# Performance work log

Measured on AMD Instinct MI355X. Metric: run time of the kernel, lower is better.

The kernel has to match this reference:

```python
import jax, jax.numpy as jnp
import numpy as np

N_NODES = 10000
N_EDGES = 640000
D_IN = 128
D_INTER = 128


def gcn_conv(x, edge_index, edge_weight, W, b):
    # PyG GCNConv: out = D^{-1/2} (A + I) D^{-1/2} (X W) + b
    n = x.shape[0]
    h = x @ W  # [N, D_out]
    row, col = edge_index[0], edge_index[1]  # source, target
    loop = jnp.arange(n, dtype=row.dtype)
    row = jnp.concatenate([row, loop])
    col = jnp.concatenate([col, loop])
    ew = jnp.concatenate([edge_weight, jnp.ones((n,), edge_weight.dtype)])
    deg = jax.ops.segment_sum(ew, col, num_segments=n)  # in-degree incl. self loops
    dinv = jnp.where(deg > 0, jax.lax.rsqrt(deg), jnp.zeros_like(deg))
    norm = dinv[row] * ew * dinv[col]  # [E+N]
    msgs = norm[:, None] * h[row]  # gather + scale
    out = jax.ops.segment_sum(msgs, col, num_segments=n)  # scatter-add aggregate
    return out + b


def setup_inputs() -> dict:
    key = jax.random.key(0)
    ks = jax.random.split(key, 8)
    x = jax.random.normal(ks[0], (N_NODES, D_IN), dtype=jnp.float32)
    edge_index = jax.random.randint(ks[1], (2, N_EDGES), 0, N_NODES, dtype=jnp.int64)
    edge_weight = jax.random.uniform(ks[2], (N_EDGES,), dtype=jnp.float32)
    # Glorot-ish init for linear weights, zeros for bias (PyG default)
    s1 = 1.0 / np.sqrt(D_IN)
    s2 = 1.0 / np.sqrt(D_INTER)
    W1 = jax.random.uniform(ks[3], (D_IN, D_INTER), jnp.float32, -s1, s1)
    b1 = jnp.zeros((D_INTER,), jnp.float32)
    W2 = jax.random.uniform(ks[4], (D_INTER, D_IN), jnp.float32, -s2, s2)
    b2 = jnp.zeros((D_IN,), jnp.float32)
    return {"x": x, "edge_index": edge_index, "edge_weight": edge_weight,
            "W1": W1, "b1": b1, "W2": W2, "b2": b2}


def reference(x, edge_index, edge_weight, W1, b1, W2, b2):
    # GCN.forward in eval mode: dropout is identity
    h = jax.nn.relu(gcn_conv(x, edge_index, edge_weight, W1, b1))
    out = jax.nn.relu(gcn_conv(h, edge_index, edge_weight, W2, b2))
    return out
```

## Files before the change

### kernel.cpp

```cpp
#include <hip/hip_runtime.h>

#define NN 10000
#define NE 640000
#define D  128
#define PAD_SHIFT 7
#define GEMM_BLOCKS ((NN + 31) / 32)
#define COUNT_BLOCKS (NE / 1024)


__global__ __launch_bounds__(256) void zero_kernel(int* __restrict__ p, int n) {
    int i = blockIdx.x * 256 + threadIdx.x;
    if (i < n) p[i] = 0;
}


__global__ __launch_bounds__(256) void fused_gemm_cs_kernel(const float* __restrict__ X,
                                                            const float* __restrict__ W,
                                                            float* __restrict__ H,
                                                            const int* __restrict__ ei,
                                                            const float* __restrict__ ew,
                                                            int* __restrict__ cnt,
                                                            int2* __restrict__ epack) {
    int bid = blockIdx.x;
    if (bid < GEMM_BLOCKS) {
        __shared__ float xs[32][D];
        int t  = threadIdx.x;
        int d  = t & 127;
        int rh = t >> 7;
        int r0 = bid * 32;
#pragma unroll
        for (int r = 0; r < 16; ++r) {
            int rr = r0 + rh * 16 + r;
            xs[rh * 16 + r][d] = (rr < NN) ? X[(size_t)rr * D + d] : 0.0f;
        }
        __syncthreads();
        float acc[16];
#pragma unroll
        for (int r = 0; r < 16; ++r) acc[r] = 0.0f;
        for (int k = 0; k < D; k += 4) {
            float w0 = W[(k + 0) * D + d];
            float w1 = W[(k + 1) * D + d];
            float w2 = W[(k + 2) * D + d];
            float w3 = W[(k + 3) * D + d];
#pragma unroll
            for (int r = 0; r < 16; ++r) {
                float4 xv = *reinterpret_cast<const float4*>(&xs[rh * 16 + r][k]);
                acc[r] = fmaf(xv.x, w0, acc[r]);
                acc[r] = fmaf(xv.y, w1, acc[r]);
                acc[r] = fmaf(xv.z, w2, acc[r]);
                acc[r] = fmaf(xv.w, w3, acc[r]);
            }
        }
#pragma unroll
        for (int r = 0; r < 16; ++r) {
            int rr = r0 + rh * 16 + r;
            if (rr < NN) H[(size_t)rr * D + d] = acc[r];
        }
    } else {
        int e0 = (bid - GEMM_BLOCKS) * 1024 + threadIdx.x;
        int   c[4], s[4];
        float w[4];
#pragma unroll
        for (int k = 0; k < 4; ++k) {
            int e = e0 + k * 256;
            c[k] = ei[NE + e];
            s[k] = ei[e];
            w[k] = ew[e];
        }
        int lr[4];
#pragma unroll
        for (int k = 0; k < 4; ++k) lr[k] = atomicAdd(&cnt[c[k]], 1);
#pragma unroll
        for (int k = 0; k < 4; ++k) {
            if (lr[k] < (1 << PAD_SHIFT)) {
                int2 v;
                v.x = s[k];
                v.y = __float_as_int(w[k]);
                epack[((size_t)c[k] << PAD_SHIFT) + lr[k]] = v;
            }
        }
    }
}


__global__ __launch_bounds__(256) void degdinv_kernel(const int* __restrict__ cnt,
                                                      const int2* __restrict__ epack,
                                                      float* __restrict__ dinv) {
    int node = blockIdx.x * 4 + (threadIdx.x >> 6);
    if (node >= NN) return;
    int lane = threadIdx.x & 63;
    int m = min(cnt[node], 1 << PAD_SHIFT);
    const int2* eb = epack + ((size_t)node << PAD_SHIFT);
    float s = 0.0f;
    for (int j = lane; j < m; j += 64) s += __int_as_float(eb[j].y);
#pragma unroll
    for (int off = 32; off; off >>= 1) s += __shfl_down(s, off);
    if (lane == 0) dinv[node] = rsqrtf(s + 1.0f);
}


__global__ __launch_bounds__(256) void gemm_kernel(const float* __restrict__ X,
                                                   const float* __restrict__ W,
                                                   float* __restrict__ H) {
    __shared__ float xs[32][D];
    int t  = threadIdx.x;
    int d  = t & 127;
    int rh = t >> 7;
    int r0 = blockIdx.x * 32;
#pragma unroll
    for (int r = 0; r < 16; ++r) {
        int rr = r0 + rh * 16 + r;
        xs[rh * 16 + r][d] = (rr < NN) ? X[(size_t)rr * D + d] : 0.0f;
    }
    __syncthreads();
    float acc[16];
#pragma unroll
    for (int r = 0; r < 16; ++r) acc[r] = 0.0f;
    for (int k = 0; k < D; k += 4) {
        float w0 = W[(k + 0) * D + d];
        float w1 = W[(k + 1) * D + d];
        float w2 = W[(k + 2) * D + d];
        float w3 = W[(k + 3) * D + d];
#pragma unroll
        for (int r = 0; r < 16; ++r) {
            float4 xv = *reinterpret_cast<const float4*>(&xs[rh * 16 + r][k]);
            acc[r] = fmaf(xv.x, w0, acc[r]);
            acc[r] = fmaf(xv.y, w1, acc[r]);
            acc[r] = fmaf(xv.z, w2, acc[r]);
            acc[r] = fmaf(xv.w, w3, acc[r]);
        }
    }
#pragma unroll
    for (int r = 0; r < 16; ++r) {
        int rr = r0 + rh * 16 + r;
        if (rr < NN) H[(size_t)rr * D + d] = acc[r];
    }
}


__global__ __launch_bounds__(64) void agg_half_kernel(const float* __restrict__ H,
                                                      const int* __restrict__ cnt,
                                                      const int2* __restrict__ epack,
                                                      const float* __restrict__ dinv,
                                                      const float* __restrict__ bias,
                                                      float* __restrict__ out) {
    __shared__ int   s_src[128];
    __shared__ float s_n[128];
    int i    = blockIdx.x;
    int slot = i & 7;
    int hh   = slot & 1;
    int c    = (i >> 3) * 4 + (slot >> 1);
    int t    = threadIdx.x;
    int d    = (hh << 6) | t;
    int m    = min(cnt[c], 1 << PAD_SHIFT);
    const int2* eb = epack + ((size_t)c << PAD_SHIFT);
    float di = dinv[c];
    for (int j = t; j < m; j += 64) {
        int2 v = eb[j];
        s_src[j] = v.x;
        s_n[j]   = dinv[v.x] * __int_as_float(v.y);
    }
    __syncthreads();
    float acc = di * H[(size_t)c * D + d];
    int jj = 0;
    for (; jj + 8 <= m; jj += 8) {
#pragma unroll
        for (int k = 0; k < 8; ++k)
            acc = fmaf(s_n[jj + k], H[(size_t)s_src[jj + k] * D + d], acc);
    }
    for (; jj < m; ++jj)
        acc = fmaf(s_n[jj], H[(size_t)s_src[jj] * D + d], acc);
    out[(size_t)c * D + d] = fmaxf(fmaf(di, acc, bias[d]), 0.0f);
}


extern "C" void kernel_launch(void* const* d_in, const int* in_sizes, int n_in,
                              void* d_out, int out_size, void* d_ws, size_t ws_size,
                              hipStream_t stream) {
    const float* x  = (const float*)d_in[0];
    const int*   ei = (const int*)  d_in[1];
    const float* ew = (const float*)d_in[2];
    const float* W1 = (const float*)d_in[3];
    const float* b1 = (const float*)d_in[4];
    const float* W2 = (const float*)d_in[5];
    const float* b2 = (const float*)d_in[6];
    float* out = (float*)d_out;

    char* ws = (char*)d_ws;
    size_t off = 0;
    auto alloc = [&](size_t bytes) {
        void* p = ws + off;
        off = (off + bytes + 255) & ~(size_t)255;
        return p;
    };
    int*   cnt   = (int*)  alloc(NN * 4);
    float* dinv  = (float*)alloc(NN * 4);
    int2*  epack = (int2*) alloc(((size_t)NN << PAD_SHIFT) * 8);
    float* h     = (float*)alloc((size_t)NN * D * 4);
    float* g     = (float*)alloc((size_t)NN * D * 4);

    zero_kernel<<<(NN + 255) / 256, 256, 0, stream>>>(cnt, NN);
    fused_gemm_cs_kernel<<<GEMM_BLOCKS + COUNT_BLOCKS, 256, 0, stream>>>(
        x, W1, h, ei, ew, cnt, epack);
    degdinv_kernel<<<(NN + 3) / 4, 256, 0, stream>>>(cnt, epack, dinv);

    agg_half_kernel<<<NN * 2, 64, 0, stream>>>(h, cnt, epack, dinv, b1, g);
    gemm_kernel    <<<(NN + 31) / 32, 256, 0, stream>>>(g, W2, h);
    agg_half_kernel<<<NN * 2, 64, 0, stream>>>(h, cnt, epack, dinv, b2, out);
}
```

Before: 137.6 us.

## Build edge buckets via per-block shared-memory histograms with batched global atomics

Replaces the per-edge global atomicAdd on the destination counters with a two-pass scheme. Each of 32 large blocks first histograms its edge slice in LDS, then reserves slot ranges with one global atomic per node, then scatters the edges into the padded buckets. The GEMM half of the fused kernel moves to 1024-thread blocks with fewer rows per thread so both roles can share one LDS union. This cuts global atomic contention, but the edge-building work now runs on only 32 blocks and reads the edge list twice. Local ranks are packed into 8 bits, which assumes no node receives more than 255 edges within one block's slice.

Measured after the change: 516.5 us. 275% more time.

```diff
diff --git a/kernel.cpp b/kernel.cpp
--- a/kernel.cpp
+++ b/kernel.cpp
@@ -4,8 +4,10 @@
 #define NE 640000
 #define D  128
 #define PAD_SHIFT 7
-#define GEMM_BLOCKS ((NN + 31) / 32)
-#define COUNT_BLOCKS (NE / 1024)
+#define GEMM_BLOCKS 313
+#define HIST_BLOCKS 32
+#define EPB (NE / HIST_BLOCKS)
+#define HSIZE 10240
 
 
 __global__ __launch_bounds__(256) void zero_kernel(int* __restrict__ p, int n) {
@@ -14,37 +16,39 @@
 }
 
 
-__global__ __launch_bounds__(256) void fused_gemm_cs_kernel(const float* __restrict__ X,
-                                                            const float* __restrict__ W,
-                                                            float* __restrict__ H,
-                                                            const int* __restrict__ ei,
-                                                            const float* __restrict__ ew,
-                                                            int* __restrict__ cnt,
-                                                            int2* __restrict__ epack) {
+union UShared {
+    float xs[32][D];
+    int   lh[HSIZE];
+};
+
+__global__ __launch_bounds__(1024) void fused_build_kernel(const float* __restrict__ X,
+                                                           const float* __restrict__ W,
+                                                           float* __restrict__ H,
+                                                           const int* __restrict__ ei,
+                                                           const float* __restrict__ ew,
+                                                           int* __restrict__ cnt,
+                                                           int2* __restrict__ epack) {
+    __shared__ UShared u;
     int bid = blockIdx.x;
+    int t   = threadIdx.x;
     if (bid < GEMM_BLOCKS) {
-        __shared__ float xs[32][D];
-        int t  = threadIdx.x;
         int d  = t & 127;
-        int rh = t >> 7;
+        int rg = t >> 7;
         int r0 = bid * 32;
-#pragma unroll
-        for (int r = 0; r < 16; ++r) {
-            int rr = r0 + rh * 16 + r;
-            xs[rh * 16 + r][d] = (rr < NN) ? X[(size_t)rr * D + d] : 0.0f;
-        }
-        __syncthreads();
-        float acc[16];
-#pragma unroll
-        for (int r = 0; r < 16; ++r) acc[r] = 0.0f;
+        for (int r = rg; r < 32; r += 8) {
+            int rr = r0 + r;
+            u.xs[r][d] = (rr < NN) ? X[(size_t)rr * D + d] : 0.0f;
+        }
+        __syncthreads();
+        float acc[4] = {0.f, 0.f, 0.f, 0.f};
         for (int k = 0; k < D; k += 4) {
             float w0 = W[(k + 0) * D + d];
             float w1 = W[(k + 1) * D + d];
             float w2 = W[(k + 2) * D + d];
             float w3 = W[(k + 3) * D + d];
 #pragma unroll
-            for (int r = 0; r < 16; ++r) {
-                float4 xv = *reinterpret_cast<const float4*>(&xs[rh * 16 + r][k]);
+            for (int r = 0; r < 4; ++r) {
+                float4 xv = *reinterpret_cast<const float4*>(&u.xs[rg * 4 + r][k]);
                 acc[r] = fmaf(xv.x, w0, acc[r]);
                 acc[r] = fmaf(xv.y, w1, acc[r]);
                 acc[r] = fmaf(xv.z, w2, acc[r]);
@@ -52,31 +56,37 @@
             }
         }
 #pragma unroll
-        for (int r = 0; r < 16; ++r) {
-            int rr = r0 + rh * 16 + r;
+        for (int r = 0; r < 4; ++r) {
+            int rr = r0 + rg * 4 + r;
             if (rr < NN) H[(size_t)rr * D + d] = acc[r];
         }
     } else {
-        int e0 = (bid - GEMM_BLOCKS) * 1024 + threadIdx.x;
-        int   c[4], s[4];
-        float w[4];
-#pragma unroll
-        for (int k = 0; k < 4; ++k) {
-            int e = e0 + k * 256;
-            c[k] = ei[NE + e];
-            s[k] = ei[e];
-            w[k] = ew[e];
-        }
-        int lr[4];
-#pragma unroll
-        for (int k = 0; k < 4; ++k) lr[k] = atomicAdd(&cnt[c[k]], 1);
-#pragma unroll
-        for (int k = 0; k < 4; ++k) {
-            if (lr[k] < (1 << PAD_SHIFT)) {
+        int bh = bid - GEMM_BLOCKS;
+        int e0 = bh * EPB;
+        for (int i = t; i < HSIZE; i += 1024) u.lh[i] = 0;
+        __syncthreads();
+        unsigned lrp[5] = {0u, 0u, 0u, 0u, 0u};
+        for (int j = t, k = 0; j < EPB; j += 1024, ++k) {
+            int c  = ei[NE + e0 + j];
+            int lr = atomicAdd(&u.lh[c], 1);
+            lrp[k >> 2] |= (unsigned)(lr & 255) << ((k & 3) * 8);
+        }
+        __syncthreads();
+        for (int i = t; i < NN; i += 1024) {
+            int hcnt = u.lh[i];
+            if (hcnt > 0) u.lh[i] = atomicAdd(&cnt[i], hcnt);
+        }
+        __syncthreads();
+        for (int j = t, k = 0; j < EPB; j += 1024, ++k) {
+            int e  = e0 + j;
+            int c  = ei[NE + e];
+            int lr = (int)((lrp[k >> 2] >> ((k & 3) * 8)) & 255u);
+            int slot = u.lh[c] + lr;
+            if (slot < (1 << PAD_SHIFT)) {
                 int2 v;
-                v.x = s[k];
-                v.y = __float_as_int(w[k]);
-                epack[((size_t)c[k] << PAD_SHIFT) + lr[k]] = v;
+                v.x = ei[e];
+                v.y = __float_as_int(ew[e]);
+                epack[((size_t)c << PAD_SHIFT) + slot] = v;
             }
         }
     }
@@ -200,7 +210,7 @@
     float* g     = (float*)alloc((size_t)NN * D * 4);
 
     zero_kernel<<<(NN + 255) / 256, 256, 0, stream>>>(cnt, NN);
-    fused_gemm_cs_kernel<<<GEMM_BLOCKS + COUNT_BLOCKS, 256, 0, stream>>>(
+    fused_build_kernel<<<GEMM_BLOCKS + HIST_BLOCKS, 1024, 0, stream>>>(
         x, W1, h, ei, ew, cnt, epack);
     degdinv_kernel<<<(NN + 3) / 4, 256, 0, stream>>>(cnt, epack, dinv);
 
```
